# Kernel optimization log

Hardware: AMD Instinct MI355X
Metric: run time of the kernel (lower is better)

## Reference

```python
import jax, jax.numpy as jnp
import numpy as np

N_HEADS = 12

def setup_inputs() -> dict:
    key = jax.random.key(0)
    k1, k2, k3 = jax.random.split(key, 3)
    B, L, D = 2, 2048, 768
    x = jax.random.normal(k1, (B, L, D), dtype=jnp.float32)
    attention_mask = jnp.ones((B, L), dtype=jnp.int32)  # 1 = real token
    w_qkv = jax.random.normal(k2, (D, 3 * D), dtype=jnp.float32) * (1.0 / np.sqrt(D))
    b_qkv = jnp.zeros((3 * D,), dtype=jnp.float32)
    w_out = jax.random.normal(k3, (D, D), dtype=jnp.float32) * (1.0 / np.sqrt(D))
    b_out = jnp.zeros((D,), dtype=jnp.float32)
    return {"x": x, "attention_mask": attention_mask, "w_qkv": w_qkv,
            "b_qkv": b_qkv, "w_out": w_out, "b_out": b_out}

def reference(x, attention_mask, w_qkv, b_qkv, w_out, b_out):
    B, L, D = x.shape
    H = N_HEADS
    dk = D // H
    # fused QKV projection
    qkv = jnp.einsum('bld,de->ble', x, w_qkv) + b_qkv  # (B,L,3D)
    q, k, v = jnp.split(qkv, 3, axis=-1)
    def to_heads(t):
        return t.reshape(B, L, H, dk).transpose(0, 2, 1, 3)  # (B,H,L,dk)
    q, k, v = to_heads(q), to_heads(k), to_heads(v)
    scale = 1.0 / jnp.sqrt(jnp.asarray(dk, dtype=x.dtype))
    scores = jnp.einsum('bhqd,bhkd->bhqk', q, k) * scale  # (B,H,L,L)
    mask = (attention_mask != 0)[:, None, None, :]  # (B,1,1,L), True = keep
    neg = jnp.asarray(jnp.finfo(scores.dtype).min, dtype=scores.dtype)
    scores = jnp.where(mask, scores, neg)
    weights = jax.nn.softmax(scores, axis=-1)
    out = jnp.einsum('bhqk,bhkd->bhqd', weights, v)  # (B,H,L,dk)
    out = out.transpose(0, 2, 1, 3).reshape(B, L, D)
    return jnp.einsum('bld,de->ble', out, w_out) + b_out
```

## Files before the change

kernel.cpp:

```cpp
#include <hip/hip_runtime.h>

typedef __bf16 bf16;
typedef bf16 bf16x4 __attribute__((ext_vector_type(4)));
typedef bf16 bf16x8 __attribute__((ext_vector_type(8)));
typedef float f32x4 __attribute__((ext_vector_type(4)));

#define MFMA16(A, B, C) __builtin_amdgcn_mfma_f32_16x16x32_bf16(A, B, C, 0, 0, 0)
#define NEG_BIG -30000.0f

#define GLOAD_LDS16(gptr, lptr)                                                \
    __builtin_amdgcn_global_load_lds(                                          \
        (__attribute__((address_space(1))) void*)(gptr),                       \
        (__attribute__((address_space(3))) void*)(lptr), 16, 0, 0)

#define SW(r, c8) ((r) * 64 + (((((c8) >> 3) ^ ((r) & 7))) << 3))
#define SW32(r, q) ((r) * 32 + ((((q) ^ ((r) & 3))) << 3))

__global__ void mark_k(float* __restrict__ out, float val, int n) {
    int i = blockIdx.x * 256 + threadIdx.x;
    if (i < n) out[i] = val;
}

__global__ __launch_bounds__(256) void cvt_x_k(const float* __restrict__ src,
                                               bf16* __restrict__ dst, int n) {
    int i = (blockIdx.x * 256 + threadIdx.x) * 8;
    if (i >= n) return;
    float4 a = *(const float4*)&src[i];
    float4 b = *(const float4*)&src[i + 4];
    bf16x8 w;
    w[0] = (bf16)a.x; w[1] = (bf16)a.y; w[2] = (bf16)a.z; w[3] = (bf16)a.w;
    w[4] = (bf16)b.x; w[5] = (bf16)b.y; w[6] = (bf16)b.z; w[7] = (bf16)b.w;
    *(bf16x8*)&dst[i] = w;
}

__global__ __launch_bounds__(256) void transpose_cvt_tiled(
    const float* __restrict__ src, bf16* __restrict__ dst, int R, int C) {
    __shared__ float t[32][33];
    int tid = threadIdx.x, tx = tid & 31, ty = tid >> 5;
    int bx = blockIdx.x * 32, by = blockIdx.y * 32;
#pragma unroll
    for (int i = 0; i < 4; ++i) {
        int row = by + ty + i * 8;
        t[ty + i * 8][tx] = src[(size_t)row * C + bx + tx];
    }
    __syncthreads();
#pragma unroll
    for (int i = 0; i < 4; ++i) {
        int outrow = bx + ty + i * 8;
        dst[(size_t)outrow * R + by + tx] = (bf16)t[tx][ty + i * 8];
    }
}

#define CLD 136

__global__ __launch_bounds__(256) void gemm_qkv_v5(
    const bf16* __restrict__ A, const bf16* __restrict__ B,
    const float* __restrict__ bias, bf16* __restrict__ Qh,
    bf16* __restrict__ Kh, bf16* __restrict__ Vth) {
    __shared__ __align__(16) bf16 SMEM[128 * CLD];
    int tid = threadIdx.x, lane = tid & 63, wave = tid >> 6;
    int quad = lane >> 4, l16 = lane & 15;
    int wr = wave >> 1, wc = wave & 1;
    int m0 = blockIdx.y * 128, n0 = blockIdx.x * 128;
    const int K = 768;
    const f32x4 fz = {0.f, 0.f, 0.f, 0.f};
    f32x4 acc[4][4];
#pragma unroll
    for (int nj = 0; nj < 4; ++nj)
#pragma unroll
        for (int mi = 0; mi < 4; ++mi) acc[nj][mi] = fz;
    const bf16* Ablk = A + (size_t)m0 * K;
    const bf16* Bblk = B + (size_t)n0 * K;
    int srow = lane >> 2, c = lane & 3;

#pragma unroll
    for (int i = 0; i < 2; ++i) {
        int r0 = i * 64 + wave * 16;
        int row = r0 + srow;
        int sc = (c ^ (row & 3)) << 3;
        GLOAD_LDS16(&Ablk[(size_t)row * K + sc], &SMEM[r0 * 32]);
        GLOAD_LDS16(&Bblk[(size_t)row * K + sc], &SMEM[4096 + r0 * 32]);
    }

    int p = 0;
    for (int k0 = 0; k0 < K; k0 += 32) {
        __syncthreads();
        if (k0 + 32 < K) {
            int kn = k0 + 32;
#pragma unroll
            for (int i = 0; i < 2; ++i) {
                int r0 = i * 64 + wave * 16;
                int row = r0 + srow;
                int sc = (c ^ (row & 3)) << 3;
                GLOAD_LDS16(&Ablk[(size_t)row * K + kn + sc],
                            &SMEM[(1 - p) * 8192 + r0 * 32]);
                GLOAD_LDS16(&Bblk[(size_t)row * K + kn + sc],
                            &SMEM[4096 + (1 - p) * 8192 + r0 * 32]);
            }
        }
        const bf16* Asp = &SMEM[p * 8192];
        const bf16* Bsp = &SMEM[4096 + p * 8192];
        bf16x8 af[4], bfv[4];
#pragma unroll
        for (int t = 0; t < 4; ++t) {
            af[t]  = *(const bf16x8*)&Asp[SW32(wr * 64 + t * 16 + l16, quad)];
            bfv[t] = *(const bf16x8*)&Bsp[SW32(wc * 64 + t * 16 + l16, quad)];
        }
#pragma unroll
        for (int nj = 0; nj < 4; ++nj)
#pragma unroll
            for (int mi = 0; mi < 4; ++mi)
                acc[nj][mi] = MFMA16(bfv[nj], af[mi], acc[nj][mi]);
        p ^= 1;
    }

    int which = n0 / 768;
    int h0 = (n0 % 768) >> 6;
    int b = m0 >> 11, l0 = m0 & 2047;
    __syncthreads();

    if (which == 2) {
#pragma unroll
        for (int nj = 0; nj < 4; ++nj) {
            int cl0 = wc * 64 + nj * 16 + quad * 4;
            float4 bv4 = *(const float4*)&bias[n0 + cl0];
            float bv[4] = {bv4.x, bv4.y, bv4.z, bv4.w};
#pragma unroll
            for (int mi = 0; mi < 4; ++mi) {
                int xrl = wr * 64 + mi * 16 + l16;
#pragma unroll
                for (int r = 0; r < 4; ++r)
                    SMEM[(cl0 + r) * CLD + xrl] = (bf16)(acc[nj][mi][r] + bv[r]);
            }
        }
    } else {
        float s = (which == 0) ? 0.18033688f : 1.0f;
#pragma unroll
        for (int nj = 0; nj < 4; ++nj) {
            int cl0 = wc * 64 + nj * 16 + quad * 4;
            float4 bv4 = *(const float4*)&bias[n0 + cl0];
            float bv[4] = {bv4.x, bv4.y, bv4.z, bv4.w};
#pragma unroll
            for (int mi = 0; mi < 4; ++mi) {
                int xrl = wr * 64 + mi * 16 + l16;
                bf16x4 v;
#pragma unroll
                for (int r = 0; r < 4; ++r) v[r] = (bf16)((acc[nj][mi][r] + bv[r]) * s);
                *(bf16x4*)&SMEM[xrl * CLD + cl0] = v;
            }
        }
    }
    __syncthreads();

    if (which == 2) {
#pragma unroll
        for (int i = 0; i < 8; ++i) {
            int idx = i * 256 + tid;
            int cl = idx >> 4, ch = idx & 15;
            int d = cl & 63, h = h0 + (cl >> 6);
            bf16x8 v = *(const bf16x8*)&SMEM[cl * CLD + ch * 8];
            *(bf16x8*)&Vth[((size_t)(b * 12 + h) * 64 + d) * 2048 + l0 + ch * 8] = v;
        }
    } else {
        bf16* dst = (which == 0) ? Qh : Kh;
#pragma unroll
        for (int i = 0; i < 8; ++i) {
            int idx = i * 256 + tid;
            int rr = idx >> 4, ch = idx & 15;
            int h = h0 + (ch >> 3), d0 = (ch & 7) * 8;
            bf16x8 v = *(const bf16x8*)&SMEM[rr * CLD + ch * 8];
            *(bf16x8*)&dst[((size_t)(b * 12 + h) * 2048 + l0 + rr) * 64 + d0] = v;
        }
    }
}

__global__ __launch_bounds__(128) void gemm_out_v4(
    const bf16* __restrict__ A, const bf16* __restrict__ B,
    const float* __restrict__ bias, float* __restrict__ C) {
    __shared__ __align__(16) bf16 As[2][128 * 32];
    __shared__ __align__(16) bf16 Bs[2][64 * 32];
    int tid = threadIdx.x, lane = tid & 63, wave = tid >> 6;
    int quad = lane >> 4, l16 = lane & 15;
    int m0 = blockIdx.y * 128, n0 = blockIdx.x * 64;
    const int K = 768, N = 768;
    const f32x4 fz = {0.f, 0.f, 0.f, 0.f};
    f32x4 acc[4][4];
#pragma unroll
    for (int mi = 0; mi < 4; ++mi)
#pragma unroll
        for (int nj = 0; nj < 4; ++nj) acc[mi][nj] = fz;
    const bf16* Ablk = A + (size_t)m0 * K;
    const bf16* Bblk = B + (size_t)n0 * K;
    int srow = lane >> 2, c = lane & 3;

#pragma unroll
    for (int i = 0; i < 4; ++i) {
        int r0 = i * 32 + wave * 16;
        int row = r0 + srow;
        int sc = (c ^ (row & 3)) << 3;
        GLOAD_LDS16(&Ablk[(size_t)row * K + sc], &As[0][r0 * 32]);
    }
#pragma unroll
    for (int i = 0; i < 2; ++i) {
        int r0 = i * 32 + wave * 16;
        int row = r0 + srow;
        int sc = (c ^ (row & 3)) << 3;
        GLOAD_LDS16(&Bblk[(size_t)row * K + sc], &Bs[0][r0 * 32]);
    }

    int p = 0;
    for (int k0 = 0; k0 < K; k0 += 32) {
        __syncthreads();
        if (k0 + 32 < K) {
            int kn = k0 + 32;
#pragma unroll
            for (int i = 0; i < 4; ++i) {
                int r0 = i * 32 + wave * 16;
                int row = r0 + srow;
                int sc = (c ^ (row & 3)) << 3;
                GLOAD_LDS16(&Ablk[(size_t)row * K + kn + sc], &As[1 - p][r0 * 32]);
            }
#pragma unroll
            for (int i = 0; i < 2; ++i) {
                int r0 = i * 32 + wave * 16;
                int row = r0 + srow;
                int sc = (c ^ (row & 3)) << 3;
                GLOAD_LDS16(&Bblk[(size_t)row * K + kn + sc], &Bs[1 - p][r0 * 32]);
            }
        }
        bf16x8 af[4], bfv[4];
#pragma unroll
        for (int t = 0; t < 4; ++t) {
            af[t]  = *(const bf16x8*)&As[p][SW32(wave * 64 + t * 16 + l16, quad)];
            bfv[t] = *(const bf16x8*)&Bs[p][SW32(t * 16 + l16, quad)];
        }
#pragma unroll
        for (int mi = 0; mi < 4; ++mi)
#pragma unroll
            for (int nj = 0; nj < 4; ++nj)
                acc[mi][nj] = MFMA16(af[mi], bfv[nj], acc[mi][nj]);
        p ^= 1;
    }

#pragma unroll
    for (int nj = 0; nj < 4; ++nj) {
        int col = n0 + nj * 16 + l16;
        float bv = bias[col];
#pragma unroll
        for (int mi = 0; mi < 4; ++mi)
#pragma unroll
            for (int r = 0; r < 4; ++r) {
                int row = m0 + wave * 64 + mi * 16 + quad * 4 + r;
                C[(size_t)row * N + col] = acc[mi][nj][r] + bv;
            }
    }
}

#define PLD 72

__global__ __launch_bounds__(256) void flash_attn(
    const bf16* __restrict__ Q, const bf16* __restrict__ K,
    const bf16* __restrict__ V, const int* __restrict__ mask,
    bf16* __restrict__ po0, bf16* __restrict__ po1, float* __restrict__ lbuf) {
    __shared__ __align__(16) bf16 Ks[2][64 * 64];
    __shared__ __align__(16) bf16 Vs[2][64 * 64];
    __shared__ __align__(16) bf16 Ps[4][16 * PLD];
    __shared__ float maskS[1024];
    __shared__ int cleanF;

    int tid = threadIdx.x, lane = tid & 63, wave = tid >> 6;
    int quad = lane >> 4, l16 = lane & 15;

    int n = blockIdx.x;
    int xcd = n & 7, idx = n >> 3;
    int g = xcd * 6 + (idx >> 4);
    int m = idx & 15;
    int bh = g % 24;
    int split = g / 24;
    int b = bh / 12;
    int s0 = split * 1024;
    int q0 = m * 128 + wave * 32;

    bf16x8 aq[2][2];
#pragma unroll
    for (int qt = 0; qt < 2; ++qt) {
        const bf16* Qp = Q + ((size_t)bh * 2048 + q0 + qt * 16 + l16) * 64;
        aq[qt][0] = *(const bf16x8*)(Qp + quad * 8);
        aq[qt][1] = *(const bf16x8*)(Qp + 32 + quad * 8);
    }

    if (tid == 0) cleanF = 1;
    __syncthreads();
    const int* mrow = mask + b * 2048 + s0;
    int myclean = 1;
#pragma unroll
    for (int i = 0; i < 4; ++i) {
        int idx2 = i * 256 + tid;
        int mv = mrow[idx2];
        maskS[idx2] = mv ? 0.0f : NEG_BIG;
        myclean &= (mv != 0);
    }
    if (!myclean) cleanF = 0;

    const f32x4 fz = {0.f, 0.f, 0.f, 0.f};
    f32x4 o[2][4];
    float l_i[2] = {0.f, 0.f};
#pragma unroll
    for (int qt = 0; qt < 2; ++qt)
#pragma unroll
        for (int dt = 0; dt < 4; ++dt) o[qt][dt] = fz;

    int srow = tid >> 3;
    int sc8  = (tid & 7) * 8;
    const bf16* Kbase = K + ((size_t)bh * 2048 + s0) * 64;
    const bf16* Vbase = V + (size_t)bh * 64 * 2048 + s0;

#pragma unroll
    for (int i = 0; i < 2; ++i) {
        int row = srow + i * 32;
        *(bf16x8*)&Ks[0][SW(row, sc8)] =
            *(const bf16x8*)&Kbase[(size_t)row * 64 + sc8];
        *(bf16x8*)&Vs[0][SW(row, sc8)] =
            *(const bf16x8*)&Vbase[(size_t)row * 2048 + sc8];
    }
    __syncthreads();
    int clean = cleanF;

    int p = 0;
    for (int kb = 0; kb < 1024; kb += 64) {
        bf16x8 kreg[2], vreg[2];
        const int pref = (kb + 64 < 1024);
        if (pref) {
            int nb = kb + 64;
#pragma unroll
            for (int i = 0; i < 2; ++i) {
                int row = srow + i * 32;
                kreg[i] = *(const bf16x8*)&Kbase[(size_t)(nb + row) * 64 + sc8];
                vreg[i] = *(const bf16x8*)&Vbase[(size_t)row * 2048 + nb + sc8];
            }
        }

        f32x4 s[2][4];
#pragma unroll
        for (int ct = 0; ct < 4; ++ct) {
            int krow = ct * 16 + l16;
            bf16x8 kf0 = *(const bf16x8*)&Ks[p][SW(krow, quad * 8)];
            bf16x8 kf1 = *(const bf16x8*)&Ks[p][SW(krow, 32 + quad * 8)];
#pragma unroll
            for (int qt = 0; qt < 2; ++qt) {
                f32x4 t = fz;
                t = MFMA16(kf0, aq[qt][0], t);
                t = MFMA16(kf1, aq[qt][1], t);
                s[qt][ct] = t;
            }
        }

        if (!clean) {
#pragma unroll
            for (int ct = 0; ct < 4; ++ct) {
                float4 mv = *(const float4*)&maskS[kb + ct * 16 + quad * 4];
                float ma[4] = {mv.x, mv.y, mv.z, mv.w};
#pragma unroll
                for (int qt = 0; qt < 2; ++qt)
#pragma unroll
                    for (int r = 0; r < 4; ++r) s[qt][ct][r] += ma[r];
            }
        }

#pragma unroll
        for (int qt = 0; qt < 2; ++qt) {
            float sum = 0.f;
#pragma unroll
            for (int ct = 0; ct < 4; ++ct)
#pragma unroll
                for (int r = 0; r < 4; ++r) {
                    float pv = __builtin_amdgcn_exp2f(s[qt][ct][r]);
                    s[qt][ct][r] = pv;
                    sum += pv;
                }
            sum += __shfl_xor(sum, 16);
            sum += __shfl_xor(sum, 32);
            l_i[qt] += sum;
        }

        bf16x8 vf[2][4];
#pragma unroll
        for (int ks = 0; ks < 2; ++ks)
#pragma unroll
            for (int dt = 0; dt < 4; ++dt)
                vf[ks][dt] = *(const bf16x8*)&Vs[p][SW(dt * 16 + l16, ks * 32 + quad * 8)];

#pragma unroll
        for (int qt = 0; qt < 2; ++qt) {
#pragma unroll
            for (int ct = 0; ct < 4; ++ct) {
                bf16x4 pk;
#pragma unroll
                for (int r = 0; r < 4; ++r) pk[r] = (bf16)s[qt][ct][r];
                *(bf16x4*)&Ps[wave][l16 * PLD + ct * 16 + quad * 4] = pk;
            }
#pragma unroll
            for (int ks = 0; ks < 2; ++ks) {
                bf16x8 ap = *(const bf16x8*)&Ps[wave][l16 * PLD + ks * 32 + quad * 8];
#pragma unroll
                for (int dt = 0; dt < 4; ++dt)
                    o[qt][dt] = MFMA16(ap, vf[ks][dt], o[qt][dt]);
            }
        }

        if (pref) {
#pragma unroll
            for (int i = 0; i < 2; ++i) {
                int row = srow + i * 32;
                *(bf16x8*)&Ks[1 - p][SW(row, sc8)] = kreg[i];
                *(bf16x8*)&Vs[1 - p][SW(row, sc8)] = vreg[i];
            }
        }
        __syncthreads();
        p ^= 1;
    }

    int h = bh % 12;
    bf16* obase = split ? po1 : po0;
#pragma unroll
    for (int qt = 0; qt < 2; ++qt) {
#pragma unroll
        for (int dt = 0; dt < 4; ++dt)
#pragma unroll
            for (int r = 0; r < 4; ++r) {
                int qrow = q0 + qt * 16 + quad * 4 + r;
                obase[((size_t)b * 2048 + qrow) * 768 + h * 64 + dt * 16 + l16] =
                    (bf16)o[qt][dt][r];
            }
        if (quad == 0) {
            int qrow = q0 + qt * 16 + l16;
            lbuf[((size_t)split * 24 + bh) * 2048 + qrow] = l_i[qt];
        }
    }
}

__global__ __launch_bounds__(256) void merge_k(
    bf16* __restrict__ ctx, const bf16* __restrict__ po1,
    const float* __restrict__ lbuf) {
    int idx = blockIdx.x * 256 + threadIdx.x;
    if (idx >= 4096 * 768 / 8) return;
    size_t i8 = (size_t)idx * 8;
    int row = (int)(i8 / 768);
    int col = (int)(i8 % 768);
    int bh = (row >> 11) * 12 + (col >> 6);
    int qrow = row & 2047;
    float l0 = lbuf[(size_t)bh * 2048 + qrow];
    float l1 = lbuf[(size_t)(24 + bh) * 2048 + qrow];
    float inv = 1.0f / (l0 + l1);
    bf16x8 v0 = *(const bf16x8*)&ctx[i8];
    bf16x8 v1 = *(const bf16x8*)&po1[i8];
    bf16x8 o;
#pragma unroll
    for (int k = 0; k < 8; ++k)
        o[k] = (bf16)(((float)v0[k] + (float)v1[k]) * inv);
    *(bf16x8*)&ctx[i8] = o;
}

extern "C" void kernel_launch(void* const* d_in, const int* in_sizes, int n_in,
                              void* d_out, int out_size, void* d_ws, size_t ws_size,
                              hipStream_t stream) {
    float* out = (float*)d_out;

    const float* x = nullptr; const int* mask = nullptr;
    const float* w_qkv = nullptr; const float* b_qkv = nullptr;
    const float* w_out = nullptr; const float* b_out = nullptr;
    int found = 0;
    for (int i = 0; i < n_in; ++i) {
        switch (in_sizes[i]) {
            case 3145728: x     = (const float*)d_in[i]; found |= 1;  break;
            case 4096:    mask  = (const int*)  d_in[i]; found |= 2;  break;
            case 1769472: w_qkv = (const float*)d_in[i]; found |= 4;  break;
            case 2304:    b_qkv = (const float*)d_in[i]; found |= 8;  break;
            case 589824:  w_out = (const float*)d_in[i]; found |= 16; break;
            case 768:     b_out = (const float*)d_in[i]; found |= 32; break;
        }
    }
    if (found != 63) {
        mark_k<<<(out_size + 255) / 256, 256, 0, stream>>>(
            out, 200.0f + (float)found, out_size);
        return;
    }

    const int M = 4096, D = 768, N3 = 2304;
    const size_t HEADS_ELEMS = (size_t)24 * 2048 * 64;

    bf16* ws    = (bf16*)d_ws;
    bf16* Kh    = ws;
    bf16* Vth   = Kh + HEADS_ELEMS;
    bf16* ctx   = Vth + HEADS_ELEMS;
    bf16* wqkvT = ctx + (size_t)M * D;
    bf16* woutT = wqkvT + (size_t)N3 * D;
    bf16* Qh    = (bf16*)d_out;
    bf16* xb    = (bf16*)d_out + HEADS_ELEMS;
    bf16* po1   = xb;
    float* lbuf = (float*)wqkvT;

    cvt_x_k<<<(M * D / 8 + 255) / 256, 256, 0, stream>>>(x, xb, M * D);
    transpose_cvt_tiled<<<dim3(2304 / 32, 768 / 32), 256, 0, stream>>>(
        w_qkv, wqkvT, 768, 2304);
    transpose_cvt_tiled<<<dim3(768 / 32, 768 / 32), 256, 0, stream>>>(
        w_out, woutT, 768, 768);

    gemm_qkv_v5<<<dim3(N3 / 128, M / 128), 256, 0, stream>>>(
        xb, wqkvT, b_qkv, Qh, Kh, Vth);

    flash_attn<<<dim3(768), 256, 0, stream>>>(
        Qh, Kh, Vth, mask, ctx, po1, lbuf);

    merge_k<<<(4096 * 768 / 8 + 255) / 256, 256, 0, stream>>>(ctx, po1, lbuf);

    gemm_out_v4<<<dim3(D / 64, M / 128), 128, 0, stream>>>(
        ctx, woutT, b_out, out);
}
```

Before: 181.4 us.

## Convert P to MFMA A-operand layout in registers via permlane swaps instead of LDS

The softmax probabilities were written to a per-wave LDS buffer and read back to turn the MFMA C-layout into the A-operand layout. They are now packed with v_cvt_pk_bf16_f32 and rearranged across lanes with v_permlane32/16_swap, which removes the Ps shared buffer and its LDS round trip. The row-sum cross-lane shuffles are also deferred from every key block to a single reduction at the end. This trades LDS traffic and shuffles for inline asm, and depends on the permlane sequence reproducing the exact layout the old LDS path produced.

```diff
diff --git a/kernel.cpp b/kernel.cpp
--- a/kernel.cpp
+++ b/kernel.cpp
@@ -256,15 +256,12 @@
     }
 }
 
-#define PLD 72
-
 __global__ __launch_bounds__(256) void flash_attn(
     const bf16* __restrict__ Q, const bf16* __restrict__ K,
     const bf16* __restrict__ V, const int* __restrict__ mask,
     bf16* __restrict__ po0, bf16* __restrict__ po1, float* __restrict__ lbuf) {
     __shared__ __align__(16) bf16 Ks[2][64 * 64];
     __shared__ __align__(16) bf16 Vs[2][64 * 64];
-    __shared__ __align__(16) bf16 Ps[4][16 * PLD];
     __shared__ float maskS[1024];
     __shared__ int cleanF;
 
@@ -367,22 +364,6 @@
             }
         }
 
-#pragma unroll
-        for (int qt = 0; qt < 2; ++qt) {
-            float sum = 0.f;
-#pragma unroll
-            for (int ct = 0; ct < 4; ++ct)
-#pragma unroll
-                for (int r = 0; r < 4; ++r) {
-                    float pv = __builtin_amdgcn_exp2f(s[qt][ct][r]);
-                    s[qt][ct][r] = pv;
-                    sum += pv;
-                }
-            sum += __shfl_xor(sum, 16);
-            sum += __shfl_xor(sum, 32);
-            l_i[qt] += sum;
-        }
-
         bf16x8 vf[2][4];
 #pragma unroll
         for (int ks = 0; ks < 2; ++ks)
@@ -393,18 +374,41 @@
 #pragma unroll
         for (int qt = 0; qt < 2; ++qt) {
 #pragma unroll
+            for (int ct = 0; ct < 4; ++ct)
+#pragma unroll
+                for (int r = 0; r < 4; ++r)
+                    s[qt][ct][r] = __builtin_amdgcn_exp2f(s[qt][ct][r]);
+            float t0 = (s[qt][0][0] + s[qt][0][1]) + (s[qt][0][2] + s[qt][0][3]);
+            float t1 = (s[qt][1][0] + s[qt][1][1]) + (s[qt][1][2] + s[qt][1][3]);
+            float t2 = (s[qt][2][0] + s[qt][2][1]) + (s[qt][2][2] + s[qt][2][3]);
+            float t3 = (s[qt][3][0] + s[qt][3][1]) + (s[qt][3][2] + s[qt][3][3]);
+            l_i[qt] += (t0 + t1) + (t2 + t3);
+
+            unsigned pk0[4], pk1[4];
+#pragma unroll
             for (int ct = 0; ct < 4; ++ct) {
-                bf16x4 pk;
-#pragma unroll
-                for (int r = 0; r < 4; ++r) pk[r] = (bf16)s[qt][ct][r];
-                *(bf16x4*)&Ps[wave][l16 * PLD + ct * 16 + quad * 4] = pk;
-            }
+                asm("v_cvt_pk_bf16_f32 %0, %1, %2"
+                    : "=v"(pk0[ct]) : "v"(s[qt][ct][0]), "v"(s[qt][ct][1]));
+                asm("v_cvt_pk_bf16_f32 %0, %1, %2"
+                    : "=v"(pk1[ct]) : "v"(s[qt][ct][2]), "v"(s[qt][ct][3]));
+            }
+
 #pragma unroll
             for (int ks = 0; ks < 2; ++ks) {
-                bf16x8 ap = *(const bf16x8*)&Ps[wave][l16 * PLD + ks * 32 + quad * 8];
+                unsigned a0 = pk0[2 * ks], c0 = pk0[2 * ks + 1];
+                unsigned b0 = pk1[2 * ks], d0 = pk1[2 * ks + 1];
+                asm("v_permlane32_swap_b32 %0, %1" : "+v"(a0), "+v"(c0));
+                asm("v_permlane16_swap_b32 %0, %1" : "+v"(a0), "+v"(c0));
+                asm("v_permlane32_swap_b32 %0, %1" : "+v"(b0), "+v"(d0));
+                asm("v_permlane16_swap_b32 %0, %1" : "+v"(b0), "+v"(d0));
+                union { unsigned u[4]; bf16x8 v; } ap;
+                ap.u[0] = a0;
+                ap.u[1] = b0;
+                ap.u[2] = c0;
+                ap.u[3] = d0;
 #pragma unroll
                 for (int dt = 0; dt < 4; ++dt)
-                    o[qt][dt] = MFMA16(ap, vf[ks][dt], o[qt][dt]);
+                    o[qt][dt] = MFMA16(ap.v, vf[ks][dt], o[qt][dt]);
             }
         }
 
@@ -424,6 +428,8 @@
     bf16* obase = split ? po1 : po0;
 #pragma unroll
     for (int qt = 0; qt < 2; ++qt) {
+        l_i[qt] += __shfl_xor(l_i[qt], 16);
+        l_i[qt] += __shfl_xor(l_i[qt], 32);
 #pragma unroll
         for (int dt = 0; dt < 4; ++dt)
 #pragma unroll
```

After: 174.3 us. -4.0%, faster.
